# Optimization experiments

Measured on AMD Instinct MI355X. Metric: run time of the kernel, lower is better.

Reference implementation:

```python
import jax, jax.numpy as jnp
import numpy as np

N_HEADS = 16

def setup_inputs() -> dict:
    key = jax.random.key(0)
    ks = jax.random.split(key, 4)
    B, T, C = 2, 2048, 1024
    scale = 0.02
    return {
        "x": jax.random.normal(ks[0], (B, T, C), dtype=jnp.float32),
        "w_qkv": jax.random.normal(ks[1], (C, 3 * C), dtype=jnp.float32) * scale,
        "b_qkv": jnp.zeros((3 * C,), dtype=jnp.float32),
        "w_out": jax.random.normal(ks[2], (C, C), dtype=jnp.float32) * scale,
        "b_out": jnp.zeros((C,), dtype=jnp.float32),
    }

def reference(x, w_qkv, b_qkv, w_out, b_out):
    B, T, C = x.shape
    H = N_HEADS
    hd = C // H
    qkv = x @ w_qkv + b_qkv                      # [B,T,3C]
    q, k, v = jnp.split(qkv, 3, axis=-1)
    # [B,H,T,hd]
    q = q.reshape(B, T, H, hd).transpose(0, 2, 1, 3)
    k = k.reshape(B, T, H, hd).transpose(0, 2, 1, 3)
    v = v.reshape(B, T, H, hd).transpose(0, 2, 1, 3)
    att = jnp.einsum('bhqd,bhkd->bhqk', q, k) / jnp.sqrt(jnp.float32(hd))
    causal = jnp.tril(jnp.ones((T, T), dtype=bool))
    att = jnp.where(causal, att, -jnp.inf)
    att = jax.nn.softmax(att, axis=-1)
    # dropout is identity in eval mode (p effectively 0 for reference)
    y = jnp.einsum('bhqk,bhkd->bhqd', att, v)
    y = y.transpose(0, 2, 1, 3).reshape(B, T, C)
    return y @ w_out + b_out
```

## Files before the change

kernel.cpp:

```cpp
#include <hip/hip_runtime.h>
#include <hip/hip_bf16.h>

#define DEVI __device__ __forceinline__

typedef __attribute__((ext_vector_type(8))) short bf16x8_t;
typedef __attribute__((ext_vector_type(4))) float f32x4_t;
typedef __attribute__((ext_vector_type(4))) short s16x4_t;
typedef __attribute__((ext_vector_type(2))) unsigned int u32x2_t;

#define QSCALE 0.18033688011112043f
#define EXP2F(x) __builtin_amdgcn_exp2f(x)

static DEVI unsigned short f2b_bits(float f) {
    unsigned int u = __float_as_uint(f);
    unsigned int r = (u + 0x7fffu + ((u >> 16) & 1u)) >> 16;
    return (unsigned short)r;
}

static DEVI unsigned int cvtpk_bf16(float lo, float hi) {
    unsigned int r;
    asm("v_cvt_pk_bf16_f32 %0, %1, %2" : "=v"(r) : "v"(lo), "v"(hi));
    return r;
}

static DEVI void gload16(const short* g, short* l) {
    __builtin_amdgcn_global_load_lds((const __attribute__((address_space(1))) void*)g,
                                     (__attribute__((address_space(3))) void*)l, 16, 0, 0);
}

#define MEMFENCE asm volatile("" ::: "memory")

__global__ __launch_bounds__(256) void prep_k(const float* __restrict__ x, short* __restrict__ xb,
                                              const float* __restrict__ wqkv, short* __restrict__ wqkvT,
                                              const float* __restrict__ wout, short* __restrict__ woutT) {
    const int bid = blockIdx.x;
    const int tid = threadIdx.x;
    if (bid < 4096) {
        const long i = ((long)bid * 256 + tid) * 4;
        const float4 v = *(const float4*)(x + i);
        s16x4_t o;
        o[0] = (short)f2b_bits(v.x); o[1] = (short)f2b_bits(v.y);
        o[2] = (short)f2b_bits(v.z); o[3] = (short)f2b_bits(v.w);
        *(s16x4_t*)(xb + i) = o;
        return;
    }
    __shared__ float tile[32][33];
    const float* w; short* wT; int K, N, bx, by;
    if (bid < 4096 + 3072) {
        const int rel = bid - 4096;
        w = wqkv; wT = wqkvT; K = 1024; N = 3072; bx = rel % 96; by = rel / 96;
    } else {
        const int rel = bid - 7168;
        w = wout; wT = woutT; K = 1024; N = 1024; bx = rel & 31; by = rel >> 5;
    }
    const int n0 = bx * 32, k0 = by * 32;
    const int tx = tid & 31, ty = tid >> 5;
#pragma unroll
    for (int i = 0; i < 4; ++i)
        tile[ty + 8 * i][tx] = w[(long)(k0 + ty + 8 * i) * N + n0 + tx];
    __syncthreads();
#pragma unroll
    for (int i = 0; i < 4; ++i)
        wT[(long)(n0 + ty + 8 * i) * K + k0 + tx] = (short)f2b_bits(tile[tx][ty + 8 * i]);
}

template<int MODE, int NF>
__global__ __launch_bounds__(256, 3) void gemm_bt(const short* __restrict__ A,
                                                  const short* __restrict__ Bt,
                                                  const float* __restrict__ bias,
                                                  void* __restrict__ Cv,
                                                  short* __restrict__ vtp,
                                                  int M, int N, int K) {
    __shared__ __align__(16) short lsA[2][128 * 32];
    __shared__ __align__(16) short lsB[2][32 * NF * 32];
    const int tid = threadIdx.x;
    const int lane = tid & 63;
    const int w = tid >> 6;
    const int wr = w >> 1, wc = w & 1;
    const int l15 = lane & 15, lg = lane >> 4;
    const long m0 = (long)blockIdx.y * 128;
    const long n0 = (long)blockIdx.x * (32 * NF);

    f32x4_t acc[4][NF] = {};

    const int srow = tid >> 2;
    const int scol = (tid & 3) * 8;
    const short* gA = A + (m0 + srow) * (long)K + scol;
    const short* gB = Bt + (n0 + srow) * (long)K + scol;

    auto STAGE = [&](int kt, int bi) {
        gload16(gA + kt,                &lsA[bi][tid * 8]);
        gload16(gA + kt + (long)64 * K, &lsA[bi][tid * 8 + 2048]);
        gload16(gB + kt,                &lsB[bi][tid * 8]);
        if (NF == 4) gload16(gB + kt + (long)64 * K, &lsB[bi][tid * 8 + 2048]);
    };

    const int nt = K >> 5;
    STAGE(0, 0);
    int buf = 0;

    for (int i = 0; i < nt; ++i) {
        if (i + 1 < nt) {
            STAGE((i + 1) << 5, buf ^ 1);
            if (NF == 4) asm volatile("s_waitcnt vmcnt(4)" ::: "memory");
            else         asm volatile("s_waitcnt vmcnt(3)" ::: "memory");
        } else {
            asm volatile("s_waitcnt vmcnt(0)" ::: "memory");
        }
        __builtin_amdgcn_s_barrier();
        MEMFENCE;
        bf16x8_t af[4], bfr[NF];
#pragma unroll
        for (int m = 0; m < 4; ++m)
            af[m] = *(const bf16x8_t*)&lsA[buf][(wr * 64 + m * 16 + l15) * 32 + lg * 8];
#pragma unroll
        for (int n = 0; n < NF; ++n)
            bfr[n] = *(const bf16x8_t*)&lsB[buf][(wc * NF * 16 + n * 16 + l15) * 32 + lg * 8];
#pragma unroll
        for (int m = 0; m < 4; ++m)
#pragma unroll
            for (int n = 0; n < NF; ++n)
                acc[m][n] = __builtin_amdgcn_mfma_f32_16x16x32_bf16(af[m], bfr[n], acc[m][n], 0, 0, 0);
        MEMFENCE;
        __builtin_amdgcn_s_barrier();
        buf ^= 1;
    }

#pragma unroll
    for (int n = 0; n < NF; ++n) {
        const int col = (int)n0 + wc * NF * 16 + n * 16 + l15;
        const float bv = bias[col];
        if (MODE == 1) {
#pragma unroll
            for (int m = 0; m < 4; ++m) {
                const long row = m0 + wr * 64 + m * 16 + lg * 4;
#pragma unroll
                for (int j = 0; j < 4; ++j)
                    ((float*)Cv)[(row + j) * N + col] = acc[m][n][j] + bv;
            }
        } else if (col < 2048) {
            const float sc = (col < 1024) ? QSCALE : 1.0f;
#pragma unroll
            for (int m = 0; m < 4; ++m) {
                const long row = m0 + wr * 64 + m * 16 + lg * 4;
#pragma unroll
                for (int j = 0; j < 4; ++j)
                    ((short*)Cv)[(row + j) * N + col] = (short)f2b_bits((acc[m][n][j] + bv) * sc);
            }
        } else {
            const int hc = col - 2048;
            const int hh = hc >> 6, dd = hc & 63;
#pragma unroll
            for (int m = 0; m < 4; ++m) {
                const long row = m0 + wr * 64 + m * 16 + lg * 4;
                const int bb = (int)(row >> 11), tt = (int)(row & 2047);
                s16x4_t pk;
#pragma unroll
                for (int j = 0; j < 4; ++j) pk[j] = (short)f2b_bits(acc[m][n][j] + bv);
                *(s16x4_t*)&vtp[((long)(bb * 16 + hh) * 64 + dd) * 2048 + tt] = pk;
            }
        }
    }
}

__global__ __launch_bounds__(512, 6) void attn_fwd(const short* __restrict__ qkv,
                                                   const short* __restrict__ vt,
                                                   short* __restrict__ y,
                                                   float* __restrict__ pwO0,
                                                   float* __restrict__ pwO1,
                                                   float* __restrict__ pwL) {
    __shared__ __align__(16) short lsK[2][64 * 64];
    __shared__ __align__(16) short lsV[2][64 * 64];
    __shared__ __align__(16) short lsP[8 * 16 * 64];
    const int bid = blockIdx.x;
    const int bh = bid & 31;
    const int pp = bid >> 5;
    int qt, j0, j1, part;
    if (pp < 8) { qt = pp; part = -1; j0 = 0; j1 = 2 * pp + 2; }
    else {
        const int k = pp - 8;
        qt = 8 + (k >> 1); part = k & 1;
        const int half = qt + 1;
        j0 = part ? half : 0;
        j1 = part ? (2 * qt + 2) : half;
    }
    const int b = bh >> 4, h = bh & 15;
    const int tid = threadIdx.x, w = tid >> 6, lane = tid & 63;
    const int l15 = lane & 15, lg = lane >> 4;
    const int lg4 = lg * 4;
    const int swz = (l15 & 7) << 4;
    const int qmin = qt * 128 + w * 16;

    const long qrow = (long)qmin + l15;
    const bf16x8_t qf0 = *(const bf16x8_t*)&qkv[((long)b * 2048 + qrow) * 3072 + h * 64 + lg * 8];
    const bf16x8_t qf1 = *(const bf16x8_t*)&qkv[((long)b * 2048 + qrow) * 3072 + h * 64 + 32 + lg * 8];

    const int srow = tid >> 3;
    const int scolb = (tid & 7) * 16;
    const int sc = (scolb ^ ((srow & 7) << 4)) >> 1;
    const short* gK = qkv + ((long)b * 2048 + srow) * 3072 + 1024 + h * 64 + sc;
    const short* gV = vt + ((long)bh * 64 + srow) * 2048 + sc;

    auto STAGE = [&](int jt, int bufi) {
        gload16(gK + (long)jt * 64 * 3072, &lsK[bufi][tid * 8]);
        gload16(gV + (long)jt * 64,        &lsV[bufi][tid * 8]);
    };

    float lrow = 0.f;
    f32x4_t oacc[4] = {};

    STAGE(j0, 0);
    int buf = 0;

    char* Pb = (char*)lsP + w * 2048 + l15 * 128;

    for (int j = j0; j < j1; ++j) {
        if (j + 1 < j1) {
            STAGE(j + 1, buf ^ 1);
            asm volatile("s_waitcnt vmcnt(2)" ::: "memory");
        } else {
            asm volatile("s_waitcnt vmcnt(0)" ::: "memory");
        }
        __builtin_amdgcn_s_barrier();
        MEMFENCE;

        const int base0 = qmin - j * 64;
        const bool active = (base0 > -16);
        if (active) {
            const bool needmask = (base0 < 63);
            const int nlim = needmask ? min(4, ((base0 + 15) >> 4) + 1) : 4;
            const char* Kb = (const char*)lsK[buf];
            const char* Vb = (const char*)lsV[buf];

            f32x4_t s[4] = {};
            __builtin_amdgcn_s_setprio(1);
#pragma unroll
            for (int kq = 0; kq < 2; ++kq) {
                const bf16x8_t qf = kq ? qf1 : qf0;
#pragma unroll
                for (int n = 0; n < 4; ++n) {
                    if (n < nlim) {
                        bf16x8_t kf = *(const bf16x8_t*)(Kb + (n * 16 + l15) * 128 + ((kq * 64 + lg * 16) ^ swz));
                        s[n] = __builtin_amdgcn_mfma_f32_16x16x32_bf16(kf, qf, s[n], 0, 0, 0);
                    }
                }
            }
            __builtin_amdgcn_s_setprio(0);

            float p[4][4];
#pragma unroll
            for (int n = 0; n < 4; ++n)
#pragma unroll
                for (int r = 0; r < 4; ++r) p[n][r] = s[n][r];

            if (needmask) {
                const int qb = base0 + l15;
#pragma unroll
                for (int n = 0; n < 4; ++n)
#pragma unroll
                    for (int r = 0; r < 4; ++r)
                        if (n * 16 + lg4 + r > qb) p[n][r] = -3e38f;
            }

            float lsum = 0.f;
#pragma unroll
            for (int n = 0; n < 4; ++n) {
                u32x2_t dw;
                if (n < nlim) {
#pragma unroll
                    for (int r = 0; r < 4; ++r) {
                        p[n][r] = EXP2F(p[n][r]);
                        lsum += p[n][r];
                    }
                    dw[0] = cvtpk_bf16(p[n][0], p[n][1]);
                    dw[1] = cvtpk_bf16(p[n][2], p[n][3]);
                } else {
                    dw[0] = 0u; dw[1] = 0u;
                }
                *(u32x2_t*)(Pb + ((n * 32 + lg * 8) ^ swz)) = dw;
            }
            lsum += __shfl_xor(lsum, 16);
            lsum += __shfl_xor(lsum, 32);
            lrow += lsum;

            asm volatile("s_waitcnt lgkmcnt(0)" ::: "memory");

            __builtin_amdgcn_s_setprio(1);
#pragma unroll
            for (int kk = 0; kk < 2; ++kk) {
                if (!(needmask && kk * 32 > base0 + 15)) {
                    bf16x8_t pf = *(const bf16x8_t*)(Pb + ((kk * 64 + lg * 16) ^ swz));
#pragma unroll
                    for (int n = 0; n < 4; ++n) {
                        bf16x8_t vf = *(const bf16x8_t*)(Vb + (n * 16 + l15) * 128 + ((kk * 64 + lg * 16) ^ swz));
                        oacc[n] = __builtin_amdgcn_mfma_f32_16x16x32_bf16(pf, vf, oacc[n], 0, 0, 0);
                    }
                }
            }
            __builtin_amdgcn_s_setprio(0);
        }
        MEMFENCE;
        __builtin_amdgcn_s_barrier();
        buf ^= 1;
    }

    if (part < 0) {
        float lr[4];
#pragma unroll
        for (int r = 0; r < 4; ++r) lr[r] = 1.0f / __shfl(lrow, lg4 + r);
#pragma unroll
        for (int n = 0; n < 4; ++n)
#pragma unroll
            for (int r = 0; r < 4; ++r)
                y[((long)b * 2048 + qmin + lg4 + r) * 1024 + h * 64 + n * 16 + l15] =
                    (short)f2b_bits(oacc[n][r] * lr[r]);
    } else {
        float* po = (part ? pwO1 : pwO0) + ((size_t)bh * 1024 + (qmin - 1024)) * 64;
#pragma unroll
        for (int n = 0; n < 4; ++n)
#pragma unroll
            for (int r = 0; r < 4; ++r)
                po[(lg4 + r) * 64 + n * 16 + l15] = oacc[n][r];
        if (lg == 0)
            pwL[(size_t)part * 32768 + bh * 1024 + (qmin + l15 - 1024)] = lrow;
    }
}

__global__ __launch_bounds__(256) void attn_combine(const float* __restrict__ pwO0,
                                                    const float* __restrict__ pwO1,
                                                    const float* __restrict__ pwL,
                                                    short* __restrict__ y) {
    const int idx = blockIdx.x * 256 + threadIdx.x;
    const int d = idx & 63;
    const int rr = idx >> 6;
    const int bh = rr >> 10, qr = rr & 1023;
    const int b = bh >> 4, h = bh & 15;
    const float l = pwL[rr] + pwL[32768 + rr];
    const float o = pwO0[(size_t)rr * 64 + d] + pwO1[(size_t)rr * 64 + d];
    y[((long)b * 2048 + 1024 + qr) * 1024 + h * 64 + d] = (short)f2b_bits(o / l);
}

extern "C" void kernel_launch(void* const* d_in, const int* in_sizes, int n_in,
                              void* d_out, int out_size, void* d_ws, size_t ws_size,
                              hipStream_t stream) {
    const float* x     = (const float*)d_in[0];
    const float* w_qkv = (const float*)d_in[1];
    const float* b_qkv = (const float*)d_in[2];
    const float* w_out = (const float*)d_in[3];
    const float* b_out = (const float*)d_in[4];

    char* ws = (char*)d_ws;
    short* xb    = (short*)(ws);
    float* pwO0  = (float*)(ws);
    short* wqkvT = (short*)(ws + (8u << 20));
    short* woutT = (short*)(ws + (14u << 20));
    short* qkvb  = (short*)(ws + (16u << 20));
    short* vt    = (short*)(ws + (40u << 20));
    short* yatt  = (short*)(ws + (48u << 20));
    float* pwO1  = (float*)(ws + (56u << 20));
    float* pwL   = (float*)(ws + (64u << 20));

    prep_k<<<8192, 256, 0, stream>>>(x, xb, w_qkv, wqkvT, w_out, woutT);
    gemm_bt<0, 4><<<dim3(24, 32), 256, 0, stream>>>(xb, wqkvT, b_qkv, (void*)qkvb, vt, 4096, 3072, 1024);
    attn_fwd<<<768, 512, 0, stream>>>(qkvb, vt, yatt, pwO0, pwO1, pwL);
    attn_combine<<<8192, 256, 0, stream>>>(pwO0, pwO1, pwL, yatt);
    gemm_bt<1, 2><<<dim3(16, 32), 256, 0, stream>>>(yatt, woutT, b_out, d_out, nullptr, 4096, 1024, 1024);
}
```

Before: 180.8 us.

## Use 32x32x16 MFMA in attention and keep P in registers via lane shuffles

The attention kernel moves from 16x16x32 MFMA with 8 waves of 16 query rows to 32x32x16 MFMA with 4 waves of 32 query rows each. The launch goes from 512 to 256 threads per block. The softmax probabilities are no longer round-tripped through LDS: they are packed to bf16 and exchanged across lane halves with shuffles to form the A operand directly. This removes the P shared buffer and its waitcnt, and halves K/V fragment reloads per query row. The trade-off is larger accumulators, more register pressure, coarser causal masking granularity and fewer waves per block.

```diff
diff --git a/kernel.cpp b/kernel.cpp
--- a/kernel.cpp
+++ b/kernel.cpp
@@ -5,6 +5,7 @@
 
 typedef __attribute__((ext_vector_type(8))) short bf16x8_t;
 typedef __attribute__((ext_vector_type(4))) float f32x4_t;
+typedef __attribute__((ext_vector_type(16))) float f32x16_t;
 typedef __attribute__((ext_vector_type(4))) short s16x4_t;
 typedef __attribute__((ext_vector_type(2))) unsigned int u32x2_t;
 
@@ -21,6 +22,12 @@
     unsigned int r;
     asm("v_cvt_pk_bf16_f32 %0, %1, %2" : "=v"(r) : "v"(lo), "v"(hi));
     return r;
+}
+
+static DEVI bf16x8_t mk8(unsigned int a0, unsigned int a1, unsigned int a2, unsigned int a3) {
+    union { unsigned int w[4]; bf16x8_t v; } u;
+    u.w[0] = a0; u.w[1] = a1; u.w[2] = a2; u.w[3] = a3;
+    return u.v;
 }
 
 static DEVI void gload16(const short* g, short* l) {
@@ -163,7 +170,7 @@
     }
 }
 
-__global__ __launch_bounds__(512, 6) void attn_fwd(const short* __restrict__ qkv,
+__global__ __launch_bounds__(256, 4) void attn_fwd(const short* __restrict__ qkv,
                                                    const short* __restrict__ vt,
                                                    short* __restrict__ y,
                                                    float* __restrict__ pwO0,
@@ -171,12 +178,11 @@
                                                    float* __restrict__ pwL) {
     __shared__ __align__(16) short lsK[2][64 * 64];
     __shared__ __align__(16) short lsV[2][64 * 64];
-    __shared__ __align__(16) short lsP[8 * 16 * 64];
     const int bid = blockIdx.x;
     const int bh = bid & 31;
     const int pp = bid >> 5;
     int qt, j0, j1, part;
-    if (pp < 8) { qt = pp; part = -1; j0 = 0; j1 = 2 * pp + 2; }
+    if (pp < 8) { qt = pp; part = -1; j0 = 0; j1 = 2 * qt + 2; }
     else {
         const int k = pp - 8;
         qt = 8 + (k >> 1); part = k & 1;
@@ -186,14 +192,17 @@
     }
     const int b = bh >> 4, h = bh & 15;
     const int tid = threadIdx.x, w = tid >> 6, lane = tid & 63;
-    const int l15 = lane & 15, lg = lane >> 4;
-    const int lg4 = lg * 4;
-    const int swz = (l15 & 7) << 4;
-    const int qmin = qt * 128 + w * 16;
-
-    const long qrow = (long)qmin + l15;
-    const bf16x8_t qf0 = *(const bf16x8_t*)&qkv[((long)b * 2048 + qrow) * 3072 + h * 64 + lg * 8];
-    const bf16x8_t qf1 = *(const bf16x8_t*)&qkv[((long)b * 2048 + qrow) * 3072 + h * 64 + 32 + lg * 8];
+    const int l31 = lane & 31;
+    const int hi = lane >> 5;
+    const int hi4 = hi * 4;
+    const int swz = (lane & 7) << 4;
+    const int qmin = qt * 128 + w * 32;
+
+    bf16x8_t qf[4];
+#pragma unroll
+    for (int ds = 0; ds < 4; ++ds)
+        qf[ds] = *(const bf16x8_t*)&qkv[((long)b * 2048 + qmin + l31) * 3072 +
+                                        h * 64 + ds * 16 + hi * 8];
 
     const int srow = tid >> 3;
     const int scolb = (tid & 7) * 16;
@@ -202,98 +211,98 @@
     const short* gV = vt + ((long)bh * 64 + srow) * 2048 + sc;
 
     auto STAGE = [&](int jt, int bufi) {
-        gload16(gK + (long)jt * 64 * 3072, &lsK[bufi][tid * 8]);
-        gload16(gV + (long)jt * 64,        &lsV[bufi][tid * 8]);
+        gload16(gK + (long)jt * 64 * 3072,             &lsK[bufi][tid * 8]);
+        gload16(gK + (long)jt * 64 * 3072 + 32 * 3072, &lsK[bufi][tid * 8 + 2048]);
+        gload16(gV + (long)jt * 64,                    &lsV[bufi][tid * 8]);
+        gload16(gV + (long)jt * 64 + 32 * 2048,        &lsV[bufi][tid * 8 + 2048]);
     };
 
     float lrow = 0.f;
-    f32x4_t oacc[4] = {};
+    f32x16_t oacc0 = {}, oacc1 = {};
 
     STAGE(j0, 0);
     int buf = 0;
-
-    char* Pb = (char*)lsP + w * 2048 + l15 * 128;
 
     for (int j = j0; j < j1; ++j) {
         if (j + 1 < j1) {
             STAGE(j + 1, buf ^ 1);
-            asm volatile("s_waitcnt vmcnt(2)" ::: "memory");
+            asm volatile("s_waitcnt vmcnt(4)" ::: "memory");
         } else {
             asm volatile("s_waitcnt vmcnt(0)" ::: "memory");
         }
         __builtin_amdgcn_s_barrier();
         MEMFENCE;
 
-        const int base0 = qmin - j * 64;
-        const bool active = (base0 > -16);
-        if (active) {
-            const bool needmask = (base0 < 63);
-            const int nlim = needmask ? min(4, ((base0 + 15) >> 4) + 1) : 4;
+        const int base_w = qmin - j * 64;
+        if (base_w > -32) {
             const char* Kb = (const char*)lsK[buf];
             const char* Vb = (const char*)lsV[buf];
-
-            f32x4_t s[4] = {};
+            const bool act1 = (base_w > 0);
+
+            f32x16_t s0 = {}, s1 = {};
             __builtin_amdgcn_s_setprio(1);
 #pragma unroll
-            for (int kq = 0; kq < 2; ++kq) {
-                const bf16x8_t qf = kq ? qf1 : qf0;
-#pragma unroll
-                for (int n = 0; n < 4; ++n) {
-                    if (n < nlim) {
-                        bf16x8_t kf = *(const bf16x8_t*)(Kb + (n * 16 + l15) * 128 + ((kq * 64 + lg * 16) ^ swz));
-                        s[n] = __builtin_amdgcn_mfma_f32_16x16x32_bf16(kf, qf, s[n], 0, 0, 0);
-                    }
+            for (int ds = 0; ds < 4; ++ds) {
+                bf16x8_t kf0 = *(const bf16x8_t*)(Kb + l31 * 128 + ((ds * 32 + hi * 16) ^ swz));
+                s0 = __builtin_amdgcn_mfma_f32_32x32x16_bf16(kf0, qf[ds], s0, 0, 0, 0);
+            }
+            if (act1) {
+#pragma unroll
+                for (int ds = 0; ds < 4; ++ds) {
+                    bf16x8_t kf1 = *(const bf16x8_t*)(Kb + (32 + l31) * 128 + ((ds * 32 + hi * 16) ^ swz));
+                    s1 = __builtin_amdgcn_mfma_f32_32x32x16_bf16(kf1, qf[ds], s1, 0, 0, 0);
                 }
             }
             __builtin_amdgcn_s_setprio(0);
 
-            float p[4][4];
-#pragma unroll
-            for (int n = 0; n < 4; ++n)
-#pragma unroll
-                for (int r = 0; r < 4; ++r) p[n][r] = s[n][r];
-
-            if (needmask) {
-                const int qb = base0 + l15;
-#pragma unroll
-                for (int n = 0; n < 4; ++n)
-#pragma unroll
-                    for (int r = 0; r < 4; ++r)
-                        if (n * 16 + lg4 + r > qb) p[n][r] = -3e38f;
-            }
-
             float lsum = 0.f;
-#pragma unroll
-            for (int n = 0; n < 4; ++n) {
-                u32x2_t dw;
-                if (n < nlim) {
-#pragma unroll
-                    for (int r = 0; r < 4; ++r) {
-                        p[n][r] = EXP2F(p[n][r]);
-                        lsum += p[n][r];
-                    }
-                    dw[0] = cvtpk_bf16(p[n][0], p[n][1]);
-                    dw[1] = cvtpk_bf16(p[n][2], p[n][3]);
-                } else {
-                    dw[0] = 0u; dw[1] = 0u;
+            bf16x8_t pa0[2], pa1[2];
+#pragma unroll
+            for (int sb = 0; sb < 2; ++sb) {
+                if (sb == 1 && !act1) break;
+                const f32x16_t& sv = sb ? s1 : s0;
+                const int base = base_w - sb * 32;
+                const bool nm = (base < 31);
+                float p[16];
+#pragma unroll
+                for (int r = 0; r < 16; ++r) {
+                    float x = sv[r];
+                    if (nm && ((r & 3) + 8 * (r >> 2) + hi4 > base + l31)) x = -3e38f;
+                    x = EXP2F(x);
+                    lsum += x;
+                    p[r] = x;
                 }
-                *(u32x2_t*)(Pb + ((n * 32 + lg * 8) ^ swz)) = dw;
-            }
-            lsum += __shfl_xor(lsum, 16);
+                unsigned int w0 = cvtpk_bf16(p[0], p[1]),  w1 = cvtpk_bf16(p[2], p[3]);
+                unsigned int w2 = cvtpk_bf16(p[4], p[5]),  w3 = cvtpk_bf16(p[6], p[7]);
+                unsigned int w4 = cvtpk_bf16(p[8], p[9]),  w5 = cvtpk_bf16(p[10], p[11]);
+                unsigned int w6 = cvtpk_bf16(p[12], p[13]), w7 = cvtpk_bf16(p[14], p[15]);
+                unsigned int t0 = __shfl_xor(w0, 32), t1 = __shfl_xor(w1, 32);
+                unsigned int t2 = __shfl_xor(w2, 32), t3 = __shfl_xor(w3, 32);
+                unsigned int t4 = __shfl_xor(w4, 32), t5 = __shfl_xor(w5, 32);
+                unsigned int t6 = __shfl_xor(w6, 32), t7 = __shfl_xor(w7, 32);
+                bf16x8_t f0 = mk8(hi ? t2 : w0, hi ? t3 : w1, hi ? w2 : t0, hi ? w3 : t1);
+                bf16x8_t f1 = mk8(hi ? t6 : w4, hi ? t7 : w5, hi ? w6 : t4, hi ? w7 : t5);
+                if (sb == 0) { pa0[0] = f0; pa0[1] = f1; }
+                else         { pa1[0] = f0; pa1[1] = f1; }
+            }
             lsum += __shfl_xor(lsum, 32);
             lrow += lsum;
 
-            asm volatile("s_waitcnt lgkmcnt(0)" ::: "memory");
-
             __builtin_amdgcn_s_setprio(1);
 #pragma unroll
-            for (int kk = 0; kk < 2; ++kk) {
-                if (!(needmask && kk * 32 > base0 + 15)) {
-                    bf16x8_t pf = *(const bf16x8_t*)(Pb + ((kk * 64 + lg * 16) ^ swz));
-#pragma unroll
-                    for (int n = 0; n < 4; ++n) {
-                        bf16x8_t vf = *(const bf16x8_t*)(Vb + (n * 16 + l15) * 128 + ((kk * 64 + lg * 16) ^ swz));
-                        oacc[n] = __builtin_amdgcn_mfma_f32_16x16x32_bf16(pf, vf, oacc[n], 0, 0, 0);
+            for (int dsub = 0; dsub < 2; ++dsub) {
+                f32x16_t& oa = dsub ? oacc1 : oacc0;
+                const int vrow = dsub * 32 + l31;
+#pragma unroll
+                for (int ks = 0; ks < 2; ++ks) {
+                    bf16x8_t vf0 = *(const bf16x8_t*)(Vb + vrow * 128 + ((ks * 32 + hi * 16) ^ swz));
+                    oa = __builtin_amdgcn_mfma_f32_32x32x16_bf16(pa0[ks], vf0, oa, 0, 0, 0);
+                }
+                if (act1) {
+#pragma unroll
+                    for (int ks = 0; ks < 2; ++ks) {
+                        bf16x8_t vf1 = *(const bf16x8_t*)(Vb + vrow * 128 + ((64 + ks * 32 + hi * 16) ^ swz));
+                        oa = __builtin_amdgcn_mfma_f32_32x32x16_bf16(pa1[ks], vf1, oa, 0, 0, 0);
                     }
                 }
             }
@@ -305,24 +314,25 @@
     }
 
     if (part < 0) {
-        float lr[4];
-#pragma unroll
-        for (int r = 0; r < 4; ++r) lr[r] = 1.0f / __shfl(lrow, lg4 + r);
-#pragma unroll
-        for (int n = 0; n < 4; ++n)
-#pragma unroll
-            for (int r = 0; r < 4; ++r)
-                y[((long)b * 2048 + qmin + lg4 + r) * 1024 + h * 64 + n * 16 + l15] =
-                    (short)f2b_bits(oacc[n][r] * lr[r]);
+        const float linv = 1.0f / lrow;
+#pragma unroll
+        for (int r = 0; r < 16; ++r) {
+            const int crow = (r & 3) + 8 * (r >> 2) + hi4;
+            const float lr_ = __shfl(linv, crow);
+            const long row = (long)b * 2048 + qmin + crow;
+            y[row * 1024 + h * 64 + l31]      = (short)f2b_bits(oacc0[r] * lr_);
+            y[row * 1024 + h * 64 + 32 + l31] = (short)f2b_bits(oacc1[r] * lr_);
+        }
     } else {
         float* po = (part ? pwO1 : pwO0) + ((size_t)bh * 1024 + (qmin - 1024)) * 64;
 #pragma unroll
-        for (int n = 0; n < 4; ++n)
-#pragma unroll
-            for (int r = 0; r < 4; ++r)
-                po[(lg4 + r) * 64 + n * 16 + l15] = oacc[n][r];
-        if (lg == 0)
-            pwL[(size_t)part * 32768 + bh * 1024 + (qmin + l15 - 1024)] = lrow;
+        for (int r = 0; r < 16; ++r) {
+            const int crow = (r & 3) + 8 * (r >> 2) + hi4;
+            po[crow * 64 + l31]      = oacc0[r];
+            po[crow * 64 + 32 + l31] = oacc1[r];
+        }
+        if (lane < 32)
+            pwL[(size_t)part * 32768 + bh * 1024 + (qmin + lane - 1024)] = lrow;
     }
 }
 
@@ -362,7 +372,7 @@
 
     prep_k<<<8192, 256, 0, stream>>>(x, xb, w_qkv, wqkvT, w_out, woutT);
     gemm_bt<0, 4><<<dim3(24, 32), 256, 0, stream>>>(xb, wqkvT, b_qkv, (void*)qkvb, vt, 4096, 3072, 1024);
-    attn_fwd<<<768, 512, 0, stream>>>(qkvb, vt, yatt, pwO0, pwO1, pwL);
+    attn_fwd<<<768, 256, 0, stream>>>(qkvb, vt, yatt, pwO0, pwO1, pwL);
     attn_combine<<<8192, 256, 0, stream>>>(pwO0, pwO1, pwL, yatt);
     gemm_bt<1, 2><<<dim3(16, 32), 256, 0, stream>>>(yatt, woutT, b_out, d_out, nullptr, 4096, 1024, 1024);
 }
```

New measurement: 187.5 us. +3.7%, slower.
